# Kernel tuning notes

Measured on AMD Instinct MI355X. Metric: run time of the kernel, lower is better.

Reference implementation:

```python
import jax, jax.numpy as jnp
import numpy as np
from jax.ops import segment_sum

N_NODES = 50000
N_EDGES = 800000


def _gcn_layer(h, src, dst, W, b, norm_out, norm_in, activation):
    # DGL GraphConv, norm='both': scale by src out-deg^-1/2, transform, aggregate, scale by dst in-deg^-1/2
    h = h * norm_out[:, None]
    h = h @ W                              # transform first (out dim smaller) -> cheaper messages
    msg = h[src]                           # [E, d_out] irregular gather
    agg = segment_sum(msg, dst, num_segments=h.shape[0])  # [N, d_out] scatter-add
    out = agg * norm_in[:, None] + b
    if activation is not None:
        out = activation(out)
    return out


def setup_inputs() -> dict:
    key = jax.random.key(0)
    ks = jax.random.split(key, 6)
    feat = jax.random.normal(ks[0], (N_NODES, 256), dtype=jnp.float32)
    src = jax.random.randint(ks[1], (N_EDGES,), 0, N_NODES, dtype=jnp.int32)
    dst = jax.random.randint(ks[2], (N_EDGES,), 0, N_NODES, dtype=jnp.int32)
    W1 = jax.random.normal(ks[3], (256, 64), dtype=jnp.float32) * (1.0 / np.sqrt(256))
    b1 = jnp.zeros((64,), dtype=jnp.float32)
    W2 = jax.random.normal(ks[4], (64, 40), dtype=jnp.float32) * (1.0 / np.sqrt(64))
    b2 = jnp.zeros((40,), dtype=jnp.float32)
    return {"feat": feat, "src": src, "dst": dst, "W1": W1, "b1": b1, "W2": W2, "b2": b2}


def reference(feat, src, dst, W1, b1, W2, b2):
    n = feat.shape[0]
    ones = jnp.ones((src.shape[0],), dtype=feat.dtype)
    deg_out = segment_sum(ones, src, num_segments=n)
    deg_in = segment_sum(ones, dst, num_segments=n)
    # DGL clamps degrees to min 1 (allow_zero_in_degree=True)
    norm_out = jnp.maximum(deg_out, 1.0) ** -0.5
    norm_in = jnp.maximum(deg_in, 1.0) ** -0.5
    h = _gcn_layer(feat, src, dst, W1, b1, norm_out, norm_in, jax.nn.relu)
    # dropout is identity in inference
    h = _gcn_layer(h, src, dst, W2, b2, norm_out, norm_in, None)
    return h
```

## Files before the change

kernel.cpp:

```cpp
#include <hip/hip_runtime.h>
#include <stdint.h>

#define N_NODES 50000
#define N_EDGES 800000
#define D_IN    256
#define D_H     64
#define D_O     40

#define NB_H   256
#define NT_H   512
#define EPB    (N_EDGES / NB_H)
#define BINS_W 12500
#define NBLK1  ((BINS_W + 255) / 256)

typedef unsigned int u32;
typedef unsigned short u16;
typedef unsigned char u8;
typedef __bf16 bf16;
typedef __attribute__((ext_vector_type(8))) __bf16 bf16x8;
typedef __attribute__((ext_vector_type(4))) float f32x4;


__global__ void __launch_bounds__(NT_H) hist_both_kernel(const int* __restrict__ src,
                                                         const int* __restrict__ dst,
                                                         u32* __restrict__ part_s,
                                                         u32* __restrict__ part_d,
                                                         const float* __restrict__ W1,
                                                         bf16* __restrict__ W1t) {
    __shared__ u32 bins[BINS_W];
    const int gb = blockIdx.x;
    if (gb >= 2 * NB_H) {
        int t = (gb - 2 * NB_H) * NT_H + threadIdx.x;
        int c = t & 63;
        int kq = t >> 6;
        int k0 = kq * 8;
        bf16x8 H;
#pragma unroll
        for (int j = 0; j < 8; ++j)
            H[j] = (bf16)W1[(size_t)(k0 + j) * D_H + c];
        *(bf16x8*)&W1t[(size_t)kq * 512 + c * 8] = H;
        return;
    }
    const int b = (gb < NB_H) ? gb : gb - NB_H;
    const int* __restrict__ idx = (gb < NB_H) ? src : dst;
    u32* __restrict__ part = (gb < NB_H) ? part_s : part_d;
    const int e0 = b * EPB;
    const int e1 = (e0 + EPB < N_EDGES) ? e0 + EPB : N_EDGES;
    for (int i = threadIdx.x; i < BINS_W; i += NT_H) bins[i] = 0;
    __syncthreads();
    for (int e = e0 + threadIdx.x; e < e1; e += NT_H) {
        int v = idx[e];
        atomicAdd(&bins[v >> 2], 1u << ((v & 3) * 8));
    }
    __syncthreads();
    for (int i = threadIdx.x; i < BINS_W; i += NT_H)
        part[(size_t)b * BINS_W + i] = bins[i];
}


__global__ void norm_both_kernel(const u32* __restrict__ part_s,
                                 u32* __restrict__ part_d,
                                 float* __restrict__ norm_out,
                                 float* __restrict__ norm_in,
                                 int* __restrict__ start,
                                 int* __restrict__ blocksum) {
    __shared__ int tmp[256];
    const int tid = threadIdx.x;
    if (blockIdx.x < NBLK1) {
        const int n4 = blockIdx.x * 256 + tid;
        if (n4 >= BINS_W) return;
        u32 a02 = 0, a13 = 0;
#pragma unroll 8
        for (int b = 0; b < NB_H; ++b) {
            u32 w = part_s[(size_t)b * BINS_W + n4];
            a02 += w & 0x00FF00FFu;
            a13 += (w >> 8) & 0x00FF00FFu;
        }
        float4 no;
        no.x = rsqrtf(fmaxf((float)(a02 & 0xFFFFu), 1.0f));
        no.y = rsqrtf(fmaxf((float)(a13 & 0xFFFFu), 1.0f));
        no.z = rsqrtf(fmaxf((float)(a02 >> 16), 1.0f));
        no.w = rsqrtf(fmaxf((float)(a13 >> 16), 1.0f));
        *(float4*)&norm_out[(size_t)n4 * 4] = no;
    } else {
        const int blk = blockIdx.x - NBLK1;
        const int n4 = blk * 256 + tid;
        const bool ok = (n4 < BINS_W);
        u32 a02 = 0, a13 = 0;
        if (ok) {
#pragma unroll 8
            for (int b = 0; b < NB_H; ++b) {
                size_t i = (size_t)b * BINS_W + n4;
                u32 w = part_d[i];
                u32 off = (a02 & 0xFFu) | ((a13 & 0xFFu) << 8) |
                          (a02 & 0xFF0000u) | ((a13 & 0xFF0000u) << 8);
                part_d[i] = off;
                a02 += w & 0x00FF00FFu;
                a13 += (w >> 8) & 0x00FF00FFu;
            }
        }
        const int d0 = (int)(a02 & 0xFFFFu), d1 = (int)(a13 & 0xFFFFu);
        const int d2 = (int)(a02 >> 16),    d3 = (int)(a13 >> 16);
        if (ok) {
            float4 ni;
            ni.x = rsqrtf(fmaxf((float)d0, 1.0f));
            ni.y = rsqrtf(fmaxf((float)d1, 1.0f));
            ni.z = rsqrtf(fmaxf((float)d2, 1.0f));
            ni.w = rsqrtf(fmaxf((float)d3, 1.0f));
            *(float4*)&norm_in[(size_t)n4 * 4] = ni;
        }
        int s = ok ? (d0 + d1 + d2 + d3) : 0;
        tmp[tid] = s;
        __syncthreads();
        for (int off = 1; off < 256; off <<= 1) {
            int t = (tid >= off) ? tmp[tid - off] : 0;
            __syncthreads();
            tmp[tid] += t;
            __syncthreads();
        }
        if (ok) {
            int P = tmp[tid] - s;
            int4 st;
            st.x = P;
            st.y = P + d0;
            st.z = P + d0 + d1;
            st.w = P + d0 + d1 + d2;
            *(int4*)&start[(size_t)n4 * 4] = st;
        }
        if (tid == 255) blocksum[blk] = tmp[255];
    }
}


__global__ void scan23_kernel(int* __restrict__ start, const int* __restrict__ blocksum) {
    __shared__ int pre[NBLK1];
    if (threadIdx.x == 0) {
        int a = 0;
        for (int b = 0; b < NBLK1; ++b) { pre[b] = a; a += blocksum[b]; }
    }
    __syncthreads();
    const int add = pre[blockIdx.x];
    const int n4 = blockIdx.x * 256 + threadIdx.x;
    if (n4 < BINS_W) {
        int4 v = *(int4*)&start[(size_t)n4 * 4];
        v.x += add; v.y += add; v.z += add; v.w += add;
        *(int4*)&start[(size_t)n4 * 4] = v;
    }
    if (blockIdx.x == 0 && threadIdx.x == 0) start[N_NODES] = N_EDGES;
}


__global__ void __launch_bounds__(NT_H) scatter2_kernel(const int* __restrict__ src,
                                                        const int* __restrict__ dst,
                                                        const int* __restrict__ start,
                                                        const u8* __restrict__ off8,
                                                        u16* __restrict__ ssrc) {
    __shared__ u32 cur[BINS_W];
    const int b = blockIdx.x;
    const int e0 = b * EPB;
    const int e1 = (e0 + EPB < N_EDGES) ? e0 + EPB : N_EDGES;
    for (int i = threadIdx.x; i < BINS_W; i += NT_H) cur[i] = 0;
    __syncthreads();
    for (int e = e0 + threadIdx.x; e < e1; e += NT_H) {
        int d = dst[e];
        int sh = (d & 3) * 8;
        u32 old = atomicAdd(&cur[d >> 2], 1u << sh);
        int c = (int)((old >> sh) & 0xFFu);
        int pos = start[d] + (int)off8[(size_t)b * N_NODES + d] + c;
        ssrc[pos] = (u16)src[e];
    }
}


#define AST 40

__global__ void __launch_bounds__(256, 4) gemm1_kernel(const float* __restrict__ feat,
                                                       const bf16* __restrict__ W1t,
                                                       const float* __restrict__ norm_out,
                                                       bf16* __restrict__ h1) {
    __shared__ __align__(16) bf16 Ah[2][64 * AST];
    __shared__ __align__(16) bf16 Al[2][64 * AST];
    __shared__ __align__(16) bf16 Wh[2][64 * AST];

    const int tid = threadIdx.x;
    const int lane = tid & 63;
    const int wv = __builtin_amdgcn_readfirstlane(tid >> 6);
    const int n0 = blockIdx.x * 64;

    const int ar = tid >> 2;
    const int ak = (tid & 3) * 8;
    int nra = n0 + ar; if (nra >= N_NODES) nra = N_NODES - 1;
    const float* asrc = feat + (size_t)nra * D_IN + ak;

    const int wcol = tid & 63;
    const int wk0 = (tid >> 6) * 8;
    const int wkq = tid >> 6;

    f32x4 acc[4];
#pragma unroll
    for (int ct = 0; ct < 4; ++ct) acc[ct] = (f32x4){0.f, 0.f, 0.f, 0.f};

    const int fr = lane & 15;
    const int fg = (lane >> 4) * 8;

    auto stageA = [&](int buf, int s) {
        float4 a0 = *(const float4*)(asrc + s * 32);
        float4 a1 = *(const float4*)(asrc + s * 32 + 4);
        float av[8] = {a0.x, a0.y, a0.z, a0.w, a1.x, a1.y, a1.z, a1.w};
        bf16x8 H, L;
#pragma unroll
        for (int j = 0; j < 8; ++j) {
            bf16 h = (bf16)av[j];
            H[j] = h;
            L[j] = (bf16)(av[j] - (float)h);
        }
        *(bf16x8*)&Ah[buf][ar * AST + ak] = H;
        *(bf16x8*)&Al[buf][ar * AST + ak] = L;
    };

    auto stageW = [&](int buf, int s) {
        *(bf16x8*)&Wh[buf][wcol * AST + wk0] =
            *(const bf16x8*)(W1t + ((size_t)(s * 4 + wkq) * 512 + wcol * 8));
    };

    auto compute = [&](int buf) {
        bf16x8 ah = *(const bf16x8*)&Ah[buf][(wv * 16 + fr) * AST + fg];
        bf16x8 al = *(const bf16x8*)&Al[buf][(wv * 16 + fr) * AST + fg];
#pragma unroll
        for (int ct = 0; ct < 4; ++ct) {
            bf16x8 bh = *(const bf16x8*)&Wh[buf][(ct * 16 + fr) * AST + fg];
            acc[ct] = __builtin_amdgcn_mfma_f32_16x16x32_bf16(ah, bh, acc[ct], 0, 0, 0);
            acc[ct] = __builtin_amdgcn_mfma_f32_16x16x32_bf16(al, bh, acc[ct], 0, 0, 0);
        }
    };

    stageA(0, 0);
    stageW(0, 0);
    __syncthreads();
#pragma unroll
    for (int s = 0; s < 8; ++s) {
        const int buf = s & 1;
        if (s < 7) {
            stageA(buf ^ 1, s + 1);
            stageW(buf ^ 1, s + 1);
        }
        compute(buf);
        __syncthreads();
    }

    const int orow = n0 + wv * 16 + (lane >> 4) * 4;
    const int ocol = lane & 15;
    float nrm[4];
#pragma unroll
    for (int r = 0; r < 4; ++r)
        nrm[r] = (orow + r < N_NODES) ? norm_out[orow + r] : 0.0f;
#pragma unroll
    for (int ct = 0; ct < 4; ++ct) {
#pragma unroll
        for (int r = 0; r < 4; ++r) {
            if (orow + r < N_NODES)
                h1[(size_t)(orow + r) * D_H + ct * 16 + ocol] = (bf16)(acc[ct][r] * nrm[r]);
        }
    }
}


__global__ void __launch_bounds__(256) agg1_kernel(const int* __restrict__ start,
                                                   const u16* __restrict__ ssrc,
                                                   const bf16* __restrict__ h1,
                                                   const float* __restrict__ norm_in,
                                                   const float* __restrict__ norm_out,
                                                   const float* __restrict__ b1,
                                                   bf16* __restrict__ g) {
    const int lane = threadIdx.x & 63;
    const int c = lane & 7;
    const int t = lane >> 3;
    const int n = (int)((blockIdx.x * blockDim.x + threadIdx.x) >> 6);
    if (n >= N_NODES) return;

    int beg = __builtin_amdgcn_readfirstlane(start[n]);
    int end = __builtin_amdgcn_readfirstlane(start[n + 1]);
    float acc[8];
#pragma unroll
    for (int j = 0; j < 8; ++j) acc[j] = 0.0f;

    for (int e = beg + t; e < end; e += 16) {
        int s0 = ssrc[e];
        bf16x8 v0 = *(const bf16x8*)(h1 + (size_t)s0 * D_H + c * 8);
        if (e + 8 < end) {
            int s1 = ssrc[e + 8];
            bf16x8 v1 = *(const bf16x8*)(h1 + (size_t)s1 * D_H + c * 8);
#pragma unroll
            for (int j = 0; j < 8; ++j) acc[j] += (float)v1[j];
        }
#pragma unroll
        for (int j = 0; j < 8; ++j) acc[j] += (float)v0[j];
    }
#pragma unroll
    for (int j = 0; j < 8; ++j) {
        acc[j] += __shfl_xor(acc[j], 8);
        acc[j] += __shfl_xor(acc[j], 16);
        acc[j] += __shfl_xor(acc[j], 32);
    }
    if (t == 0) {
        float ni = norm_in[n], no = norm_out[n];
        float4 b0 = *(const float4*)&b1[c * 8];
        float4 b1v = *(const float4*)&b1[c * 8 + 4];
        bf16x8 r;
        r[0] = (bf16)(fmaxf(fmaf(acc[0], ni, b0.x), 0.f) * no);
        r[1] = (bf16)(fmaxf(fmaf(acc[1], ni, b0.y), 0.f) * no);
        r[2] = (bf16)(fmaxf(fmaf(acc[2], ni, b0.z), 0.f) * no);
        r[3] = (bf16)(fmaxf(fmaf(acc[3], ni, b0.w), 0.f) * no);
        r[4] = (bf16)(fmaxf(fmaf(acc[4], ni, b1v.x), 0.f) * no);
        r[5] = (bf16)(fmaxf(fmaf(acc[5], ni, b1v.y), 0.f) * no);
        r[6] = (bf16)(fmaxf(fmaf(acc[6], ni, b1v.z), 0.f) * no);
        r[7] = (bf16)(fmaxf(fmaf(acc[7], ni, b1v.w), 0.f) * no);
        *(bf16x8*)(g + (size_t)n * D_H + c * 8) = r;
    }
}


#define AST2 72

__global__ void __launch_bounds__(256, 4) gemm2_kernel(const bf16* __restrict__ g,
                                                       const float* __restrict__ W2,
                                                       bf16* __restrict__ h2) {
    __shared__ __align__(16) bf16 Ah[64 * AST2];
    __shared__ __align__(16) bf16 Wh[48 * AST2];
    __shared__ __align__(16) bf16 Wl[48 * AST2];

    const int tid = threadIdx.x;
    const int lane = tid & 63;
    const int wv = __builtin_amdgcn_readfirstlane(tid >> 6);
    const int n0 = blockIdx.x * 64;

    {
        const int ar = tid >> 2;
        const int ak = (tid & 3) * 16;
        int nra = n0 + ar; if (nra >= N_NODES) nra = N_NODES - 1;
        const bf16* asrc = g + (size_t)nra * D_H + ak;
        *(bf16x8*)&Ah[ar * AST2 + ak]     = *(const bf16x8*)(asrc);
        *(bf16x8*)&Ah[ar * AST2 + ak + 8] = *(const bf16x8*)(asrc + 8);
    }
    if (tid < 192) {
        const int col = tid >> 2;
        const int k0 = (tid & 3) * 16;
        float wv16[16];
#pragma unroll
        for (int j = 0; j < 16; ++j)
            wv16[j] = (col < D_O) ? W2[(size_t)(k0 + j) * D_O + col] : 0.0f;
        bf16x8 H0, L0, H1, L1;
#pragma unroll
        for (int j = 0; j < 8; ++j) {
            bf16 h = (bf16)wv16[j];
            H0[j] = h; L0[j] = (bf16)(wv16[j] - (float)h);
            bf16 hb = (bf16)wv16[j + 8];
            H1[j] = hb; L1[j] = (bf16)(wv16[j + 8] - (float)hb);
        }
        *(bf16x8*)&Wh[col * AST2 + k0] = H0;
        *(bf16x8*)&Wh[col * AST2 + k0 + 8] = H1;
        *(bf16x8*)&Wl[col * AST2 + k0] = L0;
        *(bf16x8*)&Wl[col * AST2 + k0 + 8] = L1;
    }
    __syncthreads();

    const int fr = lane & 15;
    const int fg = (lane >> 4) * 8;

    f32x4 acc[3];
#pragma unroll
    for (int ct = 0; ct < 3; ++ct) acc[ct] = (f32x4){0.f, 0.f, 0.f, 0.f};

#pragma unroll
    for (int s = 0; s < 2; ++s) {
        bf16x8 ah = *(const bf16x8*)&Ah[(wv * 16 + fr) * AST2 + s * 32 + fg];
#pragma unroll
        for (int ct = 0; ct < 3; ++ct) {
            bf16x8 bh = *(const bf16x8*)&Wh[(ct * 16 + fr) * AST2 + s * 32 + fg];
            bf16x8 bl = *(const bf16x8*)&Wl[(ct * 16 + fr) * AST2 + s * 32 + fg];
            acc[ct] = __builtin_amdgcn_mfma_f32_16x16x32_bf16(ah, bh, acc[ct], 0, 0, 0);
            acc[ct] = __builtin_amdgcn_mfma_f32_16x16x32_bf16(ah, bl, acc[ct], 0, 0, 0);
        }
    }

    const int orow = n0 + wv * 16 + (lane >> 4) * 4;
    const int ocol = lane & 15;
#pragma unroll
    for (int ct = 0; ct < 3; ++ct) {
        int col = ct * 16 + ocol;
        if (col < D_O) {
#pragma unroll
            for (int r = 0; r < 4; ++r) {
                if (orow + r < N_NODES)
                    h2[(size_t)(orow + r) * D_O + col] = (bf16)acc[ct][r];
            }
        }
    }
}


__global__ void __launch_bounds__(256) agg2_kernel(const int* __restrict__ start,
                                                   const u16* __restrict__ ssrc,
                                                   const bf16* __restrict__ h2,
                                                   const float* __restrict__ norm_in,
                                                   const float* __restrict__ b2,
                                                   float* __restrict__ out) {
    const int lane = threadIdx.x & 63;
    const int c = lane & 7;
    const int t = lane >> 3;
    const int n = (int)((blockIdx.x * blockDim.x + threadIdx.x) >> 6);
    if (n >= N_NODES) return;

    int beg = __builtin_amdgcn_readfirstlane(start[n]);
    int end = __builtin_amdgcn_readfirstlane(start[n + 1]);
    float acc[8];
#pragma unroll
    for (int j = 0; j < 8; ++j) acc[j] = 0.0f;

    if (c < 5) {
        for (int e = beg + t; e < end; e += 16) {
            int s0 = ssrc[e];
            bf16x8 v0 = *(const bf16x8*)(h2 + (size_t)s0 * D_O + c * 8);
            if (e + 8 < end) {
                int s1 = ssrc[e + 8];
                bf16x8 v1 = *(const bf16x8*)(h2 + (size_t)s1 * D_O + c * 8);
#pragma unroll
                for (int j = 0; j < 8; ++j) acc[j] += (float)v1[j];
            }
#pragma unroll
            for (int j = 0; j < 8; ++j) acc[j] += (float)v0[j];
        }
    }
#pragma unroll
    for (int j = 0; j < 8; ++j) {
        acc[j] += __shfl_xor(acc[j], 8);
        acc[j] += __shfl_xor(acc[j], 16);
        acc[j] += __shfl_xor(acc[j], 32);
    }
    if (t == 0 && c < 5) {
        float ni = norm_in[n];
        float4 b0 = *(const float4*)&b2[c * 8];
        float4 b1v = *(const float4*)&b2[c * 8 + 4];
        float* op = out + (size_t)n * D_O + c * 8;
        *(float4*)(op) = make_float4(fmaf(acc[0], ni, b0.x), fmaf(acc[1], ni, b0.y),
                                     fmaf(acc[2], ni, b0.z), fmaf(acc[3], ni, b0.w));
        *(float4*)(op + 4) = make_float4(fmaf(acc[4], ni, b1v.x), fmaf(acc[5], ni, b1v.y),
                                         fmaf(acc[6], ni, b1v.z), fmaf(acc[7], ni, b1v.w));
    }
}


static inline char* alignup(char* p, size_t a) {
    return (char*)(((uintptr_t)p + a - 1) & ~(uintptr_t)(a - 1));
}

extern "C" void kernel_launch(void* const* d_in, const int* in_sizes, int n_in,
                              void* d_out, int out_size, void* d_ws, size_t ws_size,
                              hipStream_t stream) {
    const float* feat = (const float*)d_in[0];
    const int*   src  = (const int*)d_in[1];
    const int*   dst  = (const int*)d_in[2];
    const float* W1   = (const float*)d_in[3];
    const float* b1   = (const float*)d_in[4];
    const float* W2   = (const float*)d_in[5];
    const float* b2   = (const float*)d_in[6];
    float* out = (float*)d_out;

    char* p = alignup((char*)d_ws, 256);
    int*   start    = (int*)p;    p = alignup(p + (N_NODES + 1) * 4, 256);
    int*   blocksum = (int*)p;    p = alignup(p + 256 * 4, 256);
    float* norm_out = (float*)p;  p = alignup(p + N_NODES * 4, 256);
    float* norm_in  = (float*)p;  p = alignup(p + N_NODES * 4, 256);
    bf16*  W1t      = (bf16*)p;   p = alignup(p + (size_t)D_IN * D_H * 2, 256);
    u16*   ssrc     = (u16*)p;    p = alignup(p + N_EDGES * 2, 256);
    bf16*  h1       = (bf16*)p;   p = alignup(p + (size_t)N_NODES * D_H * 2, 256);
    bf16*  g        = (bf16*)p;   p = alignup(p + (size_t)N_NODES * D_H * 2, 256);
    bf16*  h2q      = (bf16*)p;   p = alignup(p + (size_t)N_NODES * D_O * 2, 256);
    u32*   part_s   = (u32*)p;    p = alignup(p + (size_t)NB_H * BINS_W * 4, 256);
    u32*   part_d   = (u32*)p;    p = alignup(p + (size_t)NB_H * BINS_W * 4, 256);

    hist_both_kernel<<<2 * NB_H + 4, NT_H, 0, stream>>>(src, dst, part_s, part_d, W1, W1t);
    norm_both_kernel<<<2 * NBLK1, 256, 0, stream>>>(part_s, part_d, norm_out, norm_in,
                                                    start, blocksum);
    scan23_kernel<<<NBLK1, 256, 0, stream>>>(start, blocksum);

    scatter2_kernel<<<NB_H, NT_H, 0, stream>>>(src, dst, start, (const u8*)part_d, ssrc);

    gemm1_kernel<<<(N_NODES + 63) / 64, 256, 0, stream>>>(feat, W1t, norm_out, h1);
    agg1_kernel<<<(N_NODES + 3) / 4, 256, 0, stream>>>(start, ssrc, h1, norm_in, norm_out, b1, g);

    gemm2_kernel<<<(N_NODES + 63) / 64, 256, 0, stream>>>(g, W2, h2q);
    agg2_kernel<<<(N_NODES + 3) / 4, 256, 0, stream>>>(start, ssrc, h2q, norm_in, b2, out);
}
```

Measured before the change: 113.5 us.

## Fuse edge scatter and first GEMM into one heterogeneous launch

Merges the CSR scatter kernel and the layer-1 GEMM into a single launch: the first NB_H blocks do the edge scatter and the rest do 64-row GEMM tiles. The aim is to overlap the atomic-heavy scatter with the bandwidth-bound feature GEMM and save one launch. In exchange, GEMM blocks now run with 512 threads where half sit idle, and every block reserves 50 KB of dynamic LDS. Both limit occupancy for the GEMM part.

```diff
diff --git a/kernel.cpp b/kernel.cpp
--- a/kernel.cpp
+++ b/kernel.cpp
@@ -12,6 +12,7 @@
 #define EPB    (N_EDGES / NB_H)
 #define BINS_W 12500
 #define NBLK1  ((BINS_W + 255) / 256)
+#define NG1    ((N_NODES + 63) / 64)
 
 typedef unsigned int u32;
 typedef unsigned short u16;
@@ -150,51 +151,56 @@
 }
 
 
-__global__ void __launch_bounds__(NT_H) scatter2_kernel(const int* __restrict__ src,
+#define AST 40
+#define G1T (64 * AST)
+
+__global__ void __launch_bounds__(NT_H) fused_gs_kernel(const float* __restrict__ feat,
+                                                        const bf16* __restrict__ W1t,
+                                                        const float* __restrict__ norm_out,
+                                                        bf16* __restrict__ h1,
+                                                        const int* __restrict__ src,
                                                         const int* __restrict__ dst,
                                                         const int* __restrict__ start,
                                                         const u8* __restrict__ off8,
                                                         u16* __restrict__ ssrc) {
-    __shared__ u32 cur[BINS_W];
-    const int b = blockIdx.x;
-    const int e0 = b * EPB;
-    const int e1 = (e0 + EPB < N_EDGES) ? e0 + EPB : N_EDGES;
-    for (int i = threadIdx.x; i < BINS_W; i += NT_H) cur[i] = 0;
-    __syncthreads();
-    for (int e = e0 + threadIdx.x; e < e1; e += NT_H) {
-        int d = dst[e];
-        int sh = (d & 3) * 8;
-        u32 old = atomicAdd(&cur[d >> 2], 1u << sh);
-        int c = (int)((old >> sh) & 0xFFu);
-        int pos = start[d] + (int)off8[(size_t)b * N_NODES + d] + c;
-        ssrc[pos] = (u16)src[e];
-    }
-}
-
-
-#define AST 40
-
-__global__ void __launch_bounds__(256, 4) gemm1_kernel(const float* __restrict__ feat,
-                                                       const bf16* __restrict__ W1t,
-                                                       const float* __restrict__ norm_out,
-                                                       bf16* __restrict__ h1) {
-    __shared__ __align__(16) bf16 Ah[2][64 * AST];
-    __shared__ __align__(16) bf16 Al[2][64 * AST];
-    __shared__ __align__(16) bf16 Wh[2][64 * AST];
-
+    extern __shared__ __align__(16) char smem[];
     const int tid = threadIdx.x;
+
+    if ((int)blockIdx.x < NB_H) {
+        u32* cur = (u32*)smem;
+        const int b = blockIdx.x;
+        const int e0 = b * EPB;
+        const int e1 = (e0 + EPB < N_EDGES) ? e0 + EPB : N_EDGES;
+        for (int i = tid; i < BINS_W; i += NT_H) cur[i] = 0;
+        __syncthreads();
+        for (int e = e0 + tid; e < e1; e += NT_H) {
+            int d = dst[e];
+            int sh = (d & 3) * 8;
+            u32 old = atomicAdd(&cur[d >> 2], 1u << sh);
+            int c = (int)((old >> sh) & 0xFFu);
+            int pos = start[d] + (int)off8[(size_t)b * N_NODES + d] + c;
+            ssrc[pos] = (u16)src[e];
+        }
+        return;
+    }
+
+    bf16* AhB = (bf16*)smem;
+    bf16* AlB = AhB + 2 * G1T;
+    bf16* WhB = AlB + 2 * G1T;
+
+    const bool act = (tid < 256);
     const int lane = tid & 63;
     const int wv = __builtin_amdgcn_readfirstlane(tid >> 6);
-    const int n0 = blockIdx.x * 64;
+    const int n0 = ((int)blockIdx.x - NB_H) * 64;
 
     const int ar = tid >> 2;
     const int ak = (tid & 3) * 8;
-    int nra = n0 + ar; if (nra >= N_NODES) nra = N_NODES - 1;
+    int nra = n0 + (ar & 63); if (nra >= N_NODES) nra = N_NODES - 1;
     const float* asrc = feat + (size_t)nra * D_IN + ak;
 
     const int wcol = tid & 63;
-    const int wk0 = (tid >> 6) * 8;
     const int wkq = tid >> 6;
+    const int wk0 = wkq * 8;
 
     f32x4 acc[4];
 #pragma unroll
@@ -214,52 +220,55 @@
             H[j] = h;
             L[j] = (bf16)(av[j] - (float)h);
         }
-        *(bf16x8*)&Ah[buf][ar * AST + ak] = H;
-        *(bf16x8*)&Al[buf][ar * AST + ak] = L;
+        *(bf16x8*)&AhB[buf * G1T + ar * AST + ak] = H;
+        *(bf16x8*)&AlB[buf * G1T + ar * AST + ak] = L;
     };
 
     auto stageW = [&](int buf, int s) {
-        *(bf16x8*)&Wh[buf][wcol * AST + wk0] =
+        *(bf16x8*)&WhB[buf * G1T + wcol * AST + wk0] =
             *(const bf16x8*)(W1t + ((size_t)(s * 4 + wkq) * 512 + wcol * 8));
     };
 
     auto compute = [&](int buf) {
-        bf16x8 ah = *(const bf16x8*)&Ah[buf][(wv * 16 + fr) * AST + fg];
-        bf16x8 al = *(const bf16x8*)&Al[buf][(wv * 16 + fr) * AST + fg];
+        bf16x8 ah = *(const bf16x8*)&AhB[buf * G1T + (wv * 16 + fr) * AST + fg];
+        bf16x8 al = *(const bf16x8*)&AlB[buf * G1T + (wv * 16 + fr) * AST + fg];
 #pragma unroll
         for (int ct = 0; ct < 4; ++ct) {
-            bf16x8 bh = *(const bf16x8*)&Wh[buf][(ct * 16 + fr) * AST + fg];
+            bf16x8 bh = *(const bf16x8*)&WhB[buf * G1T + (ct * 16 + fr) * AST + fg];
             acc[ct] = __builtin_amdgcn_mfma_f32_16x16x32_bf16(ah, bh, acc[ct], 0, 0, 0);
             acc[ct] = __builtin_amdgcn_mfma_f32_16x16x32_bf16(al, bh, acc[ct], 0, 0, 0);
         }
     };
 
-    stageA(0, 0);
-    stageW(0, 0);
+    if (act) { stageA(0, 0); stageW(0, 0); }
     __syncthreads();
 #pragma unroll
     for (int s = 0; s < 8; ++s) {
         const int buf = s & 1;
-        if (s < 7) {
-            stageA(buf ^ 1, s + 1);
-            stageW(buf ^ 1, s + 1);
-        }
-        compute(buf);
+        if (act) {
+            if (s < 7) {
+                stageA(buf ^ 1, s + 1);
+                stageW(buf ^ 1, s + 1);
+            }
+            compute(buf);
+        }
         __syncthreads();
     }
 
-    const int orow = n0 + wv * 16 + (lane >> 4) * 4;
-    const int ocol = lane & 15;
-    float nrm[4];
-#pragma unroll
-    for (int r = 0; r < 4; ++r)
-        nrm[r] = (orow + r < N_NODES) ? norm_out[orow + r] : 0.0f;
-#pragma unroll
-    for (int ct = 0; ct < 4; ++ct) {
-#pragma unroll
-        for (int r = 0; r < 4; ++r) {
-            if (orow + r < N_NODES)
-                h1[(size_t)(orow + r) * D_H + ct * 16 + ocol] = (bf16)(acc[ct][r] * nrm[r]);
+    if (act) {
+        const int orow = n0 + wv * 16 + (lane >> 4) * 4;
+        const int ocol = lane & 15;
+        float nrm[4];
+#pragma unroll
+        for (int r = 0; r < 4; ++r)
+            nrm[r] = (orow + r < N_NODES) ? norm_out[orow + r] : 0.0f;
+#pragma unroll
+        for (int ct = 0; ct < 4; ++ct) {
+#pragma unroll
+            for (int r = 0; r < 4; ++r) {
+                if (orow + r < N_NODES)
+                    h1[(size_t)(orow + r) * D_H + ct * 16 + ocol] = (bf16)(acc[ct][r] * nrm[r]);
+            }
         }
     }
 }
@@ -484,9 +493,10 @@
                                                     start, blocksum);
     scan23_kernel<<<NBLK1, 256, 0, stream>>>(start, blocksum);
 
-    scatter2_kernel<<<NB_H, NT_H, 0, stream>>>(src, dst, start, (const u8*)part_d, ssrc);
-
-    gemm1_kernel<<<(N_NODES + 63) / 64, 256, 0, stream>>>(feat, W1t, norm_out, h1);
+    fused_gs_kernel<<<NB_H + NG1, NT_H, 50176, stream>>>(feat, W1t, norm_out, h1,
+                                                         src, dst, start,
+                                                         (const u8*)part_d, ssrc);
+
     agg1_kernel<<<(N_NODES + 3) / 4, 256, 0, stream>>>(start, ssrc, h1, norm_in, norm_out, b1, g);
 
     gemm2_kernel<<<(N_NODES + 63) / 64, 256, 0, stream>>>(g, W2, h2q);
```

Result: no change. 114.3 us (+0.7%).
